# Optimization experiments

Measured on AMD Instinct MI355X. Metric: run time of the kernel, lower is better.

## Reference

```python
import jax, jax.numpy as jnp
import numpy as np

N = 8192      # nodes
E = 524288    # edges
F_IN = 256
H = 2         # heads
F_OUT = 128   # per-head out channels
LN_EPS = 1e-5
NEG_SLOPE = 0.2


def setup_inputs() -> dict:
    key = jax.random.key(0)
    ks = jax.random.split(key, 12)
    s = 0.05
    inp = {
        "x": jax.random.normal(ks[0], (N, F_IN), jnp.float32),
        "edge_index": jax.random.randint(ks[1], (2, E), 0, N, jnp.int32),
        "W_gat": jax.random.normal(ks[2], (F_IN, H * F_OUT), jnp.float32) * s,
        "att_src": jax.random.normal(ks[3], (H, F_OUT), jnp.float32) * s,
        "att_dst": jax.random.normal(ks[4], (H, F_OUT), jnp.float32) * s,
        "bias_gat": jnp.zeros((H * F_OUT,), jnp.float32),
        "w_a": jax.random.normal(ks[5], (256, 128), jnp.float32) * s,
        "b_a": jnp.zeros((128,), jnp.float32),
        "g_a": jnp.ones((128,), jnp.float32),
        "be_a": jnp.zeros((128,), jnp.float32),
        "w1": jax.random.normal(ks[6], (128, 64), jnp.float32) * s,
        "b1": jnp.zeros((64,), jnp.float32),
        "g1": jnp.ones((64,), jnp.float32),
        "be1": jnp.zeros((64,), jnp.float32),
        "w2": jax.random.normal(ks[7], (64, 32), jnp.float32) * s,
        "b2": jnp.zeros((32,), jnp.float32),
        "g2": jnp.ones((32,), jnp.float32),
        "be2": jnp.zeros((32,), jnp.float32),
        "w3": jax.random.normal(ks[8], (32, 3), jnp.float32) * s,
        "b3": jnp.zeros((3,), jnp.float32),
    }
    return inp


def _layernorm(x, g, b):
    mu = jnp.mean(x, axis=-1, keepdims=True)
    var = jnp.mean(jnp.square(x - mu), axis=-1, keepdims=True)
    return (x - mu) * jax.lax.rsqrt(var + LN_EPS) * g + b


def _gat_conv(x, edge_index, W, a_src, a_dst, bias):
    # PyG GATConv with add_self_loops=True, concat=True, dropout=0
    loop = jnp.arange(N, dtype=edge_index.dtype)
    src = jnp.concatenate([edge_index[0], loop])  # [E+N]
    dst = jnp.concatenate([edge_index[1], loop])
    h = (x @ W).reshape(N, H, F_OUT)              # per-node transform
    a_s = jnp.sum(h * a_src, axis=-1)             # [N,H]
    a_d = jnp.sum(h * a_dst, axis=-1)             # [N,H]
    e = jax.nn.leaky_relu(a_s[src] + a_d[dst], NEG_SLOPE)  # [E+N,H]
    # segment softmax over incoming edges of each dst node
    emax = jax.ops.segment_max(e, dst, num_segments=N)
    ex = jnp.exp(e - emax[dst])
    denom = jax.ops.segment_sum(ex, dst, num_segments=N)
    alpha = ex / (denom[dst] + 1e-16)             # [E+N,H]
    msg = h[src] * alpha[:, :, None]              # [E+N,H,F_OUT]
    out = jax.ops.segment_sum(msg, dst, num_segments=N)
    return out.reshape(N, H * F_OUT) + bias


def _safe_cdist(z):
    sq = jnp.sum(z * z, axis=-1)                  # [N]
    d2 = sq[:, None] + sq[None, :] - 2.0 * (z @ z.T)
    d2 = jnp.maximum(d2, 0.0)
    pos = d2 > 0
    return jnp.where(pos, jnp.sqrt(jnp.where(pos, d2, 1.0)), 0.0)


def reference(x, edge_index, W_gat, att_src, att_dst, bias_gat,
              w_a, b_a, g_a, be_a, w1, b1, g1, be1,
              w2, b2, g2, be2, w3, b3):
    h = _gat_conv(x, edge_index, W_gat, att_src, att_dst, bias_gat)
    h = jax.nn.relu(h)
    h = jax.nn.relu(_layernorm(h @ w_a + b_a, g_a, be_a))
    h = jax.nn.relu(_layernorm(h @ w1 + b1, g1, be1))
    h = jax.nn.relu(_layernorm(h @ w2 + b2, g2, be2))
    h = h @ w3 + b3                               # [N,3]
    return _safe_cdist(h)                         # [N,N]
```

## Files before the change

kernel.cpp:

```cpp
#include <hip/hip_runtime.h>
#include <hip/hip_bf16.h>

#define N_NODES 8192
#define E_EDGES 524288
#define F_IN    256
#define NH      2
#define F_OUT   128
#define C0      256

typedef float f32x4 __attribute__((ext_vector_type(4)));

__global__ __launch_bounds__(256) void gemm_xw_k(const float* __restrict__ A,
                                                 const float* __restrict__ B,
                                                 float* __restrict__ C) {
  const int K = 256, NC = 256;
  __shared__ float As[16][68];
  __shared__ float Bs[16][68];
  int bm = blockIdx.y * 64;
  int bn = blockIdx.x * 64;
  int tid = threadIdx.x;
  int tm = (tid >> 4) << 2;
  int tn = (tid & 15) << 2;
  float acc[4][4] = {};
  for (int k0 = 0; k0 < K; k0 += 16) {
#pragma unroll
    for (int i = 0; i < 4; i++) {
      int idx = tid + i * 256;
      int m = idx >> 4, k = idx & 15;
      As[k][m] = A[(bm + m) * K + k0 + k];
    }
#pragma unroll
    for (int i = 0; i < 4; i++) {
      int idx = tid + i * 256;
      int k = idx >> 6, n = idx & 63;
      Bs[k][n] = B[(k0 + k) * NC + bn + n];
    }
    __syncthreads();
#pragma unroll
    for (int k = 0; k < 16; k++) {
      float4 a = *(const float4*)&As[k][tm];
      float4 b = *(const float4*)&Bs[k][tn];
      acc[0][0] += a.x * b.x; acc[0][1] += a.x * b.y; acc[0][2] += a.x * b.z; acc[0][3] += a.x * b.w;
      acc[1][0] += a.y * b.x; acc[1][1] += a.y * b.y; acc[1][2] += a.y * b.z; acc[1][3] += a.y * b.w;
      acc[2][0] += a.z * b.x; acc[2][1] += a.z * b.y; acc[2][2] += a.z * b.z; acc[2][3] += a.z * b.w;
      acc[3][0] += a.w * b.x; acc[3][1] += a.w * b.y; acc[3][2] += a.w * b.z; acc[3][3] += a.w * b.w;
    }
    __syncthreads();
  }
#pragma unroll
  for (int i = 0; i < 4; i++) {
    float4 o = {acc[i][0], acc[i][1], acc[i][2], acc[i][3]};
    *(float4*)&C[(bm + tm + i) * NC + bn + tn] = o;
  }
}

__global__ __launch_bounds__(256) void att_scores_k(const float* __restrict__ h,
                                                    const float* __restrict__ att_src,
                                                    const float* __restrict__ att_dst,
                                                    float* __restrict__ a_s,
                                                    float* __restrict__ a_d) {
  int wave = threadIdx.x >> 6;
  int lane = threadIdx.x & 63;
  int node = blockIdx.x * 4 + wave;
  if (node >= N_NODES) return;
  const float4 hv = *(const float4*)(h + (size_t)node * C0 + lane * 4);
  const float4 vs = *(const float4*)(att_src + lane * 4);
  const float4 vd = *(const float4*)(att_dst + lane * 4);
  float s = hv.x * vs.x + hv.y * vs.y + hv.z * vs.z + hv.w * vs.w;
  float d = hv.x * vd.x + hv.y * vd.y + hv.z * vd.z + hv.w * vd.w;
#pragma unroll
  for (int off = 16; off; off >>= 1) {
    s += __shfl_xor(s, off);
    d += __shfl_xor(d, off);
  }
  if (lane == 0)  { a_s[node * 2] = s;     a_d[node * 2] = d; }
  if (lane == 32) { a_s[node * 2 + 1] = s; a_d[node * 2 + 1] = d; }
}

__global__ __launch_bounds__(256) void hist_k(const int* __restrict__ ei,
                                              int* __restrict__ deg) {
  int e = blockIdx.x * 256 + threadIdx.x;
  if (e < E_EDGES) atomicAdd(&deg[ei[E_EDGES + e]], 1);
}

__global__ __launch_bounds__(256) void scan_k(const int* __restrict__ deg,
                                              int* __restrict__ offs,
                                              int* __restrict__ cursor) {
  __shared__ int sums[256];
  int t = threadIdx.x;
  int local[32];
  int s = 0;
#pragma unroll
  for (int i = 0; i < 32; i++) { local[i] = s; s += deg[t * 32 + i]; }
  sums[t] = s;
  __syncthreads();
  for (int off = 1; off < 256; off <<= 1) {
    int u = (t >= off) ? sums[t - off] : 0;
    __syncthreads();
    if (t >= off) sums[t] += u;
    __syncthreads();
  }
  int base = sums[t] - s;
#pragma unroll
  for (int i = 0; i < 32; i++) {
    int o = base + local[i];
    offs[t * 32 + i] = o;
    cursor[t * 32 + i] = o;
  }
  if (t == 255) offs[N_NODES] = sums[255];
}

__global__ __launch_bounds__(256) void scatter_src_k(const int* __restrict__ ei,
                                                     int* __restrict__ cursor,
                                                     int* __restrict__ sorted_src) {
  int e = blockIdx.x * 256 + threadIdx.x;
  if (e < E_EDGES) {
    int d = ei[E_EDGES + e];
    int p = atomicAdd(&cursor[d], 1);
    sorted_src[p] = ei[e];
  }
}

__global__ __launch_bounds__(256) void gat_gather_k(const int* __restrict__ sorted_src,
                                                    const int* __restrict__ offs,
                                                    const float* __restrict__ h,
                                                    const float* __restrict__ a_s,
                                                    const float* __restrict__ a_d,
                                                    float* __restrict__ gat) {
  int wave = threadIdx.x >> 6;
  int lane = threadIdx.x & 63;
  int node = blockIdx.x * 4 + wave;
  if (node >= N_NODES) return;
  int start = offs[node], end = offs[node + 1];
  const float2 adv = *(const float2*)(a_d + node * 2);
  float ad0 = adv.x, ad1 = adv.y;
  int head = lane >> 5;
  float4 acc = {0, 0, 0, 0};
  float den0 = 0, den1 = 0;
  for (int base = start; base < end; base += 64) {
    int idx = base + lane;
    int s = -1;
    float e0 = 0, e1 = 0;
    if (idx < end) {
      s = sorted_src[idx];
      const float2 asv = *(const float2*)(a_s + s * 2);
      float v0 = asv.x + ad0; v0 = v0 > 0.0f ? v0 : 0.2f * v0;
      float v1 = asv.y + ad1; v1 = v1 > 0.0f ? v1 : 0.2f * v1;
      e0 = __expf(v0);
      e1 = __expf(v1);
      den0 += e0; den1 += e1;
    }
    int cnt = min(64, end - base);
    int j = 0;
    for (; j + 2 <= cnt; j += 2) {
      int sj0 = __shfl(s, j);
      int sj1 = __shfl(s, j + 1);
      float a00 = __shfl(e0, j),     a10 = __shfl(e1, j);
      float a01 = __shfl(e0, j + 1), a11 = __shfl(e1, j + 1);
      const float4 hv0 = *(const float4*)(h + (size_t)sj0 * C0 + lane * 4);
      const float4 hv1 = *(const float4*)(h + (size_t)sj1 * C0 + lane * 4);
      float w0 = head ? a10 : a00;
      float w1 = head ? a11 : a01;
      acc.x += hv0.x * w0; acc.y += hv0.y * w0; acc.z += hv0.z * w0; acc.w += hv0.w * w0;
      acc.x += hv1.x * w1; acc.y += hv1.y * w1; acc.z += hv1.z * w1; acc.w += hv1.w * w1;
    }
    if (j < cnt) {
      int sj = __shfl(s, j);
      float x0 = __shfl(e0, j);
      float x1 = __shfl(e1, j);
      float exh = head ? x1 : x0;
      const float4 hv = *(const float4*)(h + (size_t)sj * C0 + lane * 4);
      acc.x += hv.x * exh; acc.y += hv.y * exh;
      acc.z += hv.z * exh; acc.w += hv.w * exh;
    }
  }
  {
    const float2 asv = *(const float2*)(a_s + node * 2);
    float v0 = asv.x + ad0; v0 = v0 > 0.0f ? v0 : 0.2f * v0;
    float v1 = asv.y + ad1; v1 = v1 > 0.0f ? v1 : 0.2f * v1;
    float e0 = __expf(v0), e1 = __expf(v1);
    if (lane == 0) { den0 += e0; den1 += e1; }
    float exh = head ? e1 : e0;
    const float4 hv = *(const float4*)(h + (size_t)node * C0 + lane * 4);
    acc.x += hv.x * exh; acc.y += hv.y * exh;
    acc.z += hv.z * exh; acc.w += hv.w * exh;
  }
#pragma unroll
  for (int off = 32; off; off >>= 1) {
    den0 += __shfl_xor(den0, off);
    den1 += __shfl_xor(den1, off);
  }
  float denh = head ? den1 : den0;
  float inv = 1.0f / (denh + 1e-16f);
  float4 o = {acc.x * inv, acc.y * inv, acc.z * inv, acc.w * inv};
  *(float4*)(gat + (size_t)node * C0 + lane * 4) = o;
}

template <int KDIM, int ODIM, bool APPLY_IN>
__global__ __launch_bounds__(256) void fused_layer_k(const float* __restrict__ in,
                                                     const float* __restrict__ bias_in,
                                                     const float* __restrict__ W,
                                                     const float* __restrict__ b,
                                                     const float* __restrict__ g,
                                                     const float* __restrict__ be,
                                                     float* __restrict__ out) {
  const int TILE = 16;
  const int GROUPS = 256 / ODIM;
  const int NPT = TILE / GROUPS;
  __shared__ float in_t[TILE][KDIM + 4];
  __shared__ float out_t[TILE][ODIM + 1];
  int tid = threadIdx.x;
  int n0 = blockIdx.x * TILE;
  const int KD4 = KDIM / 4;
  for (int idx = tid; idx < TILE * KD4; idx += 256) {
    int n = idx / KD4, k4 = idx % KD4;
    float4 v = *(const float4*)&in[(size_t)(n0 + n) * KDIM + k4 * 4];
    if (APPLY_IN) {
      const float4 bb = *(const float4*)&bias_in[k4 * 4];
      v.x = fmaxf(v.x + bb.x, 0.0f);
      v.y = fmaxf(v.y + bb.y, 0.0f);
      v.z = fmaxf(v.z + bb.z, 0.0f);
      v.w = fmaxf(v.w + bb.w, 0.0f);
    }
    *(float4*)&in_t[n][k4 * 4] = v;
  }
  __syncthreads();
  int jj = tid % ODIM;
  int grp = tid / ODIM;
  float acc[NPT];
#pragma unroll
  for (int t = 0; t < NPT; t++) acc[t] = b[jj];
  for (int k = 0; k < KDIM; k += 4) {
    float w0 = W[(k + 0) * ODIM + jj];
    float w1 = W[(k + 1) * ODIM + jj];
    float w2 = W[(k + 2) * ODIM + jj];
    float w3 = W[(k + 3) * ODIM + jj];
#pragma unroll
    for (int t = 0; t < NPT; t++) {
      float4 v = *(const float4*)&in_t[grp + t * GROUPS][k];
      acc[t] = fmaf(v.w, w3, fmaf(v.z, w2, fmaf(v.y, w1, fmaf(v.x, w0, acc[t]))));
    }
  }
#pragma unroll
  for (int t = 0; t < NPT; t++) out_t[grp + t * GROUPS][jj] = acc[t];
  __syncthreads();
  const int TPN = 256 / TILE;
  const int JPT = ODIM / TPN;
  int node = tid / TPN;
  int ln = tid % TPN;
  float v[JPT];
  float s = 0;
#pragma unroll
  for (int q = 0; q < JPT; q++) { v[q] = out_t[node][ln + q * TPN]; s += v[q]; }
#pragma unroll
  for (int m = 1; m < TPN; m <<= 1) s += __shfl_xor(s, m);
  float mu = s / (float)ODIM;
  float vs = 0;
#pragma unroll
  for (int q = 0; q < JPT; q++) { float dd = v[q] - mu; vs += dd * dd; }
#pragma unroll
  for (int m = 1; m < TPN; m <<= 1) vs += __shfl_xor(vs, m);
  float inv = rsqrtf(vs / (float)ODIM + 1e-5f);
#pragma unroll
  for (int q = 0; q < JPT; q++) {
    int j = ln + q * TPN;
    float o = (v[q] - mu) * inv * g[j] + be[j];
    out[(size_t)(n0 + node) * ODIM + j] = fmaxf(o, 0.0f);
  }
}

__global__ __launch_bounds__(256) void final_z_k(const float* __restrict__ h2,
                                                 const float* __restrict__ w3,
                                                 const float* __restrict__ b3,
                                                 float* __restrict__ z) {
  int n = blockIdx.x * 256 + threadIdx.x;
  if (n >= N_NODES) return;
  float a0 = b3[0], a1 = b3[1], a2 = b3[2];
  const float4* row = (const float4*)(h2 + (size_t)n * 32);
#pragma unroll
  for (int q = 0; q < 8; q++) {
    float4 v = row[q];
    int k = q * 4;
    a0 += v.x * w3[(k + 0) * 3 + 0] + v.y * w3[(k + 1) * 3 + 0] + v.z * w3[(k + 2) * 3 + 0] + v.w * w3[(k + 3) * 3 + 0];
    a1 += v.x * w3[(k + 0) * 3 + 1] + v.y * w3[(k + 1) * 3 + 1] + v.z * w3[(k + 2) * 3 + 1] + v.w * w3[(k + 3) * 3 + 1];
    a2 += v.x * w3[(k + 0) * 3 + 2] + v.y * w3[(k + 1) * 3 + 2] + v.z * w3[(k + 2) * 3 + 2] + v.w * w3[(k + 3) * 3 + 2];
  }
  float4 zz = {a0, a1, a2, 0.0f};
  ((float4*)z)[n] = zz;
}

__global__ __launch_bounds__(256) void cdist_k(const float* __restrict__ z,
                                               float* __restrict__ out) {
  int i = blockIdx.x >> 3;
  int j0 = (((blockIdx.x & 7) << 8) + threadIdx.x) << 2;
  const float4 zi = ((const float4*)z)[i];
  f32x4 r;
  {
    float4 zj = ((const float4*)z)[j0 + 0];
    float dx = zi.x - zj.x, dy = zi.y - zj.y, dz = zi.z - zj.z;
    r.x = sqrtf(dx * dx + dy * dy + dz * dz);
  }
  {
    float4 zj = ((const float4*)z)[j0 + 1];
    float dx = zi.x - zj.x, dy = zi.y - zj.y, dz = zi.z - zj.z;
    r.y = sqrtf(dx * dx + dy * dy + dz * dz);
  }
  {
    float4 zj = ((const float4*)z)[j0 + 2];
    float dx = zi.x - zj.x, dy = zi.y - zj.y, dz = zi.z - zj.z;
    r.z = sqrtf(dx * dx + dy * dy + dz * dz);
  }
  {
    float4 zj = ((const float4*)z)[j0 + 3];
    float dx = zi.x - zj.x, dy = zi.y - zj.y, dz = zi.z - zj.z;
    r.w = sqrtf(dx * dx + dy * dy + dz * dz);
  }
  f32x4* dst = (f32x4*)out + (((size_t)i * N_NODES + j0) >> 2);
  __builtin_nontemporal_store(r, dst);
}

extern "C" void kernel_launch(void* const* d_in, const int* in_sizes, int n_in,
                              void* d_out, int out_size, void* d_ws, size_t ws_size,
                              hipStream_t stream) {
  const float* x        = (const float*)d_in[0];
  const int*   ei       = (const int*)d_in[1];
  const float* W_gat    = (const float*)d_in[2];
  const float* att_src  = (const float*)d_in[3];
  const float* att_dst  = (const float*)d_in[4];
  const float* bias_gat = (const float*)d_in[5];
  const float* w_a      = (const float*)d_in[6];
  const float* b_a      = (const float*)d_in[7];
  const float* g_a      = (const float*)d_in[8];
  const float* be_a     = (const float*)d_in[9];
  const float* w1       = (const float*)d_in[10];
  const float* b1       = (const float*)d_in[11];
  const float* g1       = (const float*)d_in[12];
  const float* be1      = (const float*)d_in[13];
  const float* w2       = (const float*)d_in[14];
  const float* b2       = (const float*)d_in[15];
  const float* g2       = (const float*)d_in[16];
  const float* be2      = (const float*)d_in[17];
  const float* w3       = (const float*)d_in[18];
  const float* b3       = (const float*)d_in[19];
  float* out = (float*)d_out;

  float* ws = (float*)d_ws;
  float* h     = ws;
  float* a_s   = h + 2097152;
  float* a_d   = a_s + 16384;
  float* gat   = a_d + 16384;
  float* hA    = gat + 2097152;
  float* h1    = hA + 1048576;
  float* h2    = h1 + 524288;
  float* z     = h2 + 262144;
  int*   deg    = (int*)(z + 32768);
  int*   offs   = deg + 8192;
  int*   cursor = offs + 8200;
  int*   sorted = cursor + 8192;

  hipMemsetAsync(deg, 0, N_NODES * sizeof(int), stream);

  gemm_xw_k<<<dim3(4, 128), 256, 0, stream>>>(x, W_gat, h);
  att_scores_k<<<2048, 256, 0, stream>>>(h, att_src, att_dst, a_s, a_d);
  hist_k<<<E_EDGES / 256, 256, 0, stream>>>(ei, deg);
  scan_k<<<1, 256, 0, stream>>>(deg, offs, cursor);
  scatter_src_k<<<E_EDGES / 256, 256, 0, stream>>>(ei, cursor, sorted);
  gat_gather_k<<<2048, 256, 0, stream>>>(sorted, offs, h, a_s, a_d, gat);
  fused_layer_k<256, 128, true><<<N_NODES / 16, 256, 0, stream>>>(gat, bias_gat, w_a, b_a, g_a, be_a, hA);
  fused_layer_k<128, 64, false><<<N_NODES / 16, 256, 0, stream>>>(hA, nullptr, w1, b1, g1, be1, h1);
  fused_layer_k<64, 32, false><<<N_NODES / 16, 256, 0, stream>>>(h1, nullptr, w2, b2, g2, be2, h2);
  final_z_k<<<N_NODES / 256, 256, 0, stream>>>(h2, w3, b3, z);
  cdist_k<<<N_NODES * 8, 256, 0, stream>>>(z, out);
}
```

Measured before the change: 484.8 us.

## Precompute edge attention exps in scatter and fuse final projection into last layer

The scatter kernel now handles self-loops as ordinary CSR entries, computes the leaky-relu exp weights per edge and stores them alongside the sorted source indices. The gather kernel then streams precomputed weights with wave-uniform loads instead of computing them per 64-edge chunk with shuffles, and it accumulates the denominator per lane without a reduction. Separately, the final 32-to-3 projection is fused into the last fused_layer kernel, which removes the h2 buffer and one launch. This costs an extra per-edge float2 write and read, and the gather loop now issues scalar-indexed loads serially.

```diff
diff --git a/kernel.cpp b/kernel.cpp
--- a/kernel.cpp
+++ b/kernel.cpp
@@ -7,6 +7,7 @@
 #define NH      2
 #define F_OUT   128
 #define C0      256
+#define E_TOT   (E_EDGES + N_NODES)
 
 typedef float f32x4 __attribute__((ext_vector_type(4)));
 
@@ -91,7 +92,7 @@
   int local[32];
   int s = 0;
 #pragma unroll
-  for (int i = 0; i < 32; i++) { local[i] = s; s += deg[t * 32 + i]; }
+  for (int i = 0; i < 32; i++) { local[i] = s; s += deg[t * 32 + i] + 1; }
   sums[t] = s;
   __syncthreads();
   for (int off = 1; off < 256; off <<= 1) {
@@ -110,100 +111,81 @@
   if (t == 255) offs[N_NODES] = sums[255];
 }
 
-__global__ __launch_bounds__(256) void scatter_src_k(const int* __restrict__ ei,
-                                                     int* __restrict__ cursor,
-                                                     int* __restrict__ sorted_src) {
+__global__ __launch_bounds__(256) void scatter_k(const int* __restrict__ ei,
+                                                 const float* __restrict__ a_s,
+                                                 const float* __restrict__ a_d,
+                                                 int* __restrict__ cursor,
+                                                 int* __restrict__ sorted_src,
+                                                 float2* __restrict__ exv) {
   int e = blockIdx.x * 256 + threadIdx.x;
-  if (e < E_EDGES) {
-    int d = ei[E_EDGES + e];
-    int p = atomicAdd(&cursor[d], 1);
-    sorted_src[p] = ei[e];
-  }
+  if (e >= E_TOT) return;
+  int s, d;
+  if (e < E_EDGES) { s = ei[e]; d = ei[E_EDGES + e]; }
+  else             { s = d = e - E_EDGES; }
+  const float2 as = ((const float2*)a_s)[s];
+  const float2 ad = ((const float2*)a_d)[d];
+  float v0 = as.x + ad.x; v0 = v0 > 0.0f ? v0 : 0.2f * v0;
+  float v1 = as.y + ad.y; v1 = v1 > 0.0f ? v1 : 0.2f * v1;
+  int p = atomicAdd(&cursor[d], 1);
+  sorted_src[p] = s;
+  exv[p] = make_float2(__expf(v0), __expf(v1));
 }
 
 __global__ __launch_bounds__(256) void gat_gather_k(const int* __restrict__ sorted_src,
+                                                    const float2* __restrict__ exv,
                                                     const int* __restrict__ offs,
                                                     const float* __restrict__ h,
-                                                    const float* __restrict__ a_s,
-                                                    const float* __restrict__ a_d,
                                                     float* __restrict__ gat) {
   int wave = threadIdx.x >> 6;
   int lane = threadIdx.x & 63;
   int node = blockIdx.x * 4 + wave;
   if (node >= N_NODES) return;
-  int start = offs[node], end = offs[node + 1];
-  const float2 adv = *(const float2*)(a_d + node * 2);
-  float ad0 = adv.x, ad1 = adv.y;
+  int start = __builtin_amdgcn_readfirstlane(offs[node]);
+  int end   = __builtin_amdgcn_readfirstlane(offs[node + 1]);
   int head = lane >> 5;
   float4 acc = {0, 0, 0, 0};
-  float den0 = 0, den1 = 0;
-  for (int base = start; base < end; base += 64) {
-    int idx = base + lane;
-    int s = -1;
-    float e0 = 0, e1 = 0;
-    if (idx < end) {
-      s = sorted_src[idx];
-      const float2 asv = *(const float2*)(a_s + s * 2);
-      float v0 = asv.x + ad0; v0 = v0 > 0.0f ? v0 : 0.2f * v0;
-      float v1 = asv.y + ad1; v1 = v1 > 0.0f ? v1 : 0.2f * v1;
-      e0 = __expf(v0);
-      e1 = __expf(v1);
-      den0 += e0; den1 += e1;
-    }
-    int cnt = min(64, end - base);
-    int j = 0;
-    for (; j + 2 <= cnt; j += 2) {
-      int sj0 = __shfl(s, j);
-      int sj1 = __shfl(s, j + 1);
-      float a00 = __shfl(e0, j),     a10 = __shfl(e1, j);
-      float a01 = __shfl(e0, j + 1), a11 = __shfl(e1, j + 1);
-      const float4 hv0 = *(const float4*)(h + (size_t)sj0 * C0 + lane * 4);
-      const float4 hv1 = *(const float4*)(h + (size_t)sj1 * C0 + lane * 4);
-      float w0 = head ? a10 : a00;
-      float w1 = head ? a11 : a01;
-      acc.x += hv0.x * w0; acc.y += hv0.y * w0; acc.z += hv0.z * w0; acc.w += hv0.w * w0;
-      acc.x += hv1.x * w1; acc.y += hv1.y * w1; acc.z += hv1.z * w1; acc.w += hv1.w * w1;
-    }
-    if (j < cnt) {
-      int sj = __shfl(s, j);
-      float x0 = __shfl(e0, j);
-      float x1 = __shfl(e1, j);
-      float exh = head ? x1 : x0;
-      const float4 hv = *(const float4*)(h + (size_t)sj * C0 + lane * 4);
-      acc.x += hv.x * exh; acc.y += hv.y * exh;
-      acc.z += hv.z * exh; acc.w += hv.w * exh;
-    }
-  }
-  {
-    const float2 asv = *(const float2*)(a_s + node * 2);
-    float v0 = asv.x + ad0; v0 = v0 > 0.0f ? v0 : 0.2f * v0;
-    float v1 = asv.y + ad1; v1 = v1 > 0.0f ? v1 : 0.2f * v1;
-    float e0 = __expf(v0), e1 = __expf(v1);
-    if (lane == 0) { den0 += e0; den1 += e1; }
-    float exh = head ? e1 : e0;
-    const float4 hv = *(const float4*)(h + (size_t)node * C0 + lane * 4);
-    acc.x += hv.x * exh; acc.y += hv.y * exh;
-    acc.z += hv.z * exh; acc.w += hv.w * exh;
-  }
-#pragma unroll
-  for (int off = 32; off; off >>= 1) {
-    den0 += __shfl_xor(den0, off);
-    den1 += __shfl_xor(den1, off);
-  }
-  float denh = head ? den1 : den0;
-  float inv = 1.0f / (denh + 1e-16f);
+  float den = 0.0f;
+  int e = start;
+  for (; e + 2 <= end; e += 2) {
+    int s0 = sorted_src[e];
+    int s1 = sorted_src[e + 1];
+    float2 x0 = exv[e];
+    float2 x1 = exv[e + 1];
+    const float4 hv0 = *(const float4*)(h + (size_t)s0 * C0 + lane * 4);
+    const float4 hv1 = *(const float4*)(h + (size_t)s1 * C0 + lane * 4);
+    float w0 = head ? x0.y : x0.x;
+    float w1 = head ? x1.y : x1.x;
+    den += w0; den += w1;
+    acc.x = fmaf(hv0.x, w0, acc.x); acc.y = fmaf(hv0.y, w0, acc.y);
+    acc.z = fmaf(hv0.z, w0, acc.z); acc.w = fmaf(hv0.w, w0, acc.w);
+    acc.x = fmaf(hv1.x, w1, acc.x); acc.y = fmaf(hv1.y, w1, acc.y);
+    acc.z = fmaf(hv1.z, w1, acc.z); acc.w = fmaf(hv1.w, w1, acc.w);
+  }
+  if (e < end) {
+    int s0 = sorted_src[e];
+    float2 x0 = exv[e];
+    const float4 hv0 = *(const float4*)(h + (size_t)s0 * C0 + lane * 4);
+    float w0 = head ? x0.y : x0.x;
+    den += w0;
+    acc.x = fmaf(hv0.x, w0, acc.x); acc.y = fmaf(hv0.y, w0, acc.y);
+    acc.z = fmaf(hv0.z, w0, acc.z); acc.w = fmaf(hv0.w, w0, acc.w);
+  }
+  float inv = 1.0f / (den + 1e-16f);
   float4 o = {acc.x * inv, acc.y * inv, acc.z * inv, acc.w * inv};
   *(float4*)(gat + (size_t)node * C0 + lane * 4) = o;
 }
 
-template <int KDIM, int ODIM, bool APPLY_IN>
+template <int KDIM, int ODIM, bool APPLY_IN, bool FUSE_Z>
 __global__ __launch_bounds__(256) void fused_layer_k(const float* __restrict__ in,
                                                      const float* __restrict__ bias_in,
                                                      const float* __restrict__ W,
                                                      const float* __restrict__ b,
                                                      const float* __restrict__ g,
                                                      const float* __restrict__ be,
-                                                     float* __restrict__ out) {
+                                                     float* __restrict__ out,
+                                                     const float* __restrict__ w3,
+                                                     const float* __restrict__ b3,
+                                                     float* __restrict__ zout) {
   const int TILE = 16;
   const int GROUPS = 256 / ODIM;
   const int NPT = TILE / GROUPS;
@@ -234,11 +216,11 @@
     float w0 = W[(k + 0) * ODIM + jj];
     float w1 = W[(k + 1) * ODIM + jj];
     float w2 = W[(k + 2) * ODIM + jj];
-    float w3 = W[(k + 3) * ODIM + jj];
+    float w3v = W[(k + 3) * ODIM + jj];
 #pragma unroll
     for (int t = 0; t < NPT; t++) {
       float4 v = *(const float4*)&in_t[grp + t * GROUPS][k];
-      acc[t] = fmaf(v.w, w3, fmaf(v.z, w2, fmaf(v.y, w1, fmaf(v.x, w0, acc[t]))));
+      acc[t] = fmaf(v.w, w3v, fmaf(v.z, w2, fmaf(v.y, w1, fmaf(v.x, w0, acc[t]))));
     }
   }
 #pragma unroll
@@ -261,32 +243,34 @@
 #pragma unroll
   for (int m = 1; m < TPN; m <<= 1) vs += __shfl_xor(vs, m);
   float inv = rsqrtf(vs / (float)ODIM + 1e-5f);
-#pragma unroll
-  for (int q = 0; q < JPT; q++) {
-    int j = ln + q * TPN;
-    float o = (v[q] - mu) * inv * g[j] + be[j];
-    out[(size_t)(n0 + node) * ODIM + j] = fmaxf(o, 0.0f);
-  }
-}
-
-__global__ __launch_bounds__(256) void final_z_k(const float* __restrict__ h2,
-                                                 const float* __restrict__ w3,
-                                                 const float* __restrict__ b3,
-                                                 float* __restrict__ z) {
-  int n = blockIdx.x * 256 + threadIdx.x;
-  if (n >= N_NODES) return;
-  float a0 = b3[0], a1 = b3[1], a2 = b3[2];
-  const float4* row = (const float4*)(h2 + (size_t)n * 32);
-#pragma unroll
-  for (int q = 0; q < 8; q++) {
-    float4 v = row[q];
-    int k = q * 4;
-    a0 += v.x * w3[(k + 0) * 3 + 0] + v.y * w3[(k + 1) * 3 + 0] + v.z * w3[(k + 2) * 3 + 0] + v.w * w3[(k + 3) * 3 + 0];
-    a1 += v.x * w3[(k + 0) * 3 + 1] + v.y * w3[(k + 1) * 3 + 1] + v.z * w3[(k + 2) * 3 + 1] + v.w * w3[(k + 3) * 3 + 1];
-    a2 += v.x * w3[(k + 0) * 3 + 2] + v.y * w3[(k + 1) * 3 + 2] + v.z * w3[(k + 2) * 3 + 2] + v.w * w3[(k + 3) * 3 + 2];
-  }
-  float4 zz = {a0, a1, a2, 0.0f};
-  ((float4*)z)[n] = zz;
+  if (FUSE_Z) {
+    float p0 = 0, p1 = 0, p2 = 0;
+#pragma unroll
+    for (int q = 0; q < JPT; q++) {
+      int j = ln + q * TPN;
+      float val = fmaxf((v[q] - mu) * inv * g[j] + be[j], 0.0f);
+      p0 = fmaf(val, w3[j * 3 + 0], p0);
+      p1 = fmaf(val, w3[j * 3 + 1], p1);
+      p2 = fmaf(val, w3[j * 3 + 2], p2);
+    }
+#pragma unroll
+    for (int m = 1; m < TPN; m <<= 1) {
+      p0 += __shfl_xor(p0, m);
+      p1 += __shfl_xor(p1, m);
+      p2 += __shfl_xor(p2, m);
+    }
+    if (ln == 0) {
+      float4 zz = {p0 + b3[0], p1 + b3[1], p2 + b3[2], 0.0f};
+      ((float4*)zout)[n0 + node] = zz;
+    }
+  } else {
+#pragma unroll
+    for (int q = 0; q < JPT; q++) {
+      int j = ln + q * TPN;
+      float o = (v[q] - mu) * inv * g[j] + be[j];
+      out[(size_t)(n0 + node) * ODIM + j] = fmaxf(o, 0.0f);
+    }
+  }
 }
 
 __global__ __launch_bounds__(256) void cdist_k(const float* __restrict__ z,
@@ -345,18 +329,18 @@
   float* out = (float*)d_out;
 
   float* ws = (float*)d_ws;
-  float* h     = ws;
-  float* a_s   = h + 2097152;
-  float* a_d   = a_s + 16384;
-  float* gat   = a_d + 16384;
-  float* hA    = gat + 2097152;
-  float* h1    = hA + 1048576;
-  float* h2    = h1 + 524288;
-  float* z     = h2 + 262144;
-  int*   deg    = (int*)(z + 32768);
-  int*   offs   = deg + 8192;
-  int*   cursor = offs + 8200;
-  int*   sorted = cursor + 8192;
+  float*  h      = ws;
+  float*  a_s    = h + 2097152;
+  float*  a_d    = a_s + 16384;
+  float*  gat    = a_d + 16384;
+  float*  hA     = gat + 2097152;
+  float*  h1     = hA + 1048576;
+  float*  z      = h1 + 524288;
+  float2* exv    = (float2*)(z + 32768);
+  int*    deg    = (int*)(exv + E_TOT);
+  int*    offs   = deg + 8192;
+  int*    cursor = offs + 8200;
+  int*    sorted = cursor + 8192;
 
   hipMemsetAsync(deg, 0, N_NODES * sizeof(int), stream);
 
@@ -364,11 +348,10 @@
   att_scores_k<<<2048, 256, 0, stream>>>(h, att_src, att_dst, a_s, a_d);
   hist_k<<<E_EDGES / 256, 256, 0, stream>>>(ei, deg);
   scan_k<<<1, 256, 0, stream>>>(deg, offs, cursor);
-  scatter_src_k<<<E_EDGES / 256, 256, 0, stream>>>(ei, cursor, sorted);
-  gat_gather_k<<<2048, 256, 0, stream>>>(sorted, offs, h, a_s, a_d, gat);
-  fused_layer_k<256, 128, true><<<N_NODES / 16, 256, 0, stream>>>(gat, bias_gat, w_a, b_a, g_a, be_a, hA);
-  fused_layer_k<128, 64, false><<<N_NODES / 16, 256, 0, stream>>>(hA, nullptr, w1, b1, g1, be1, h1);
-  fused_layer_k<64, 32, false><<<N_NODES / 16, 256, 0, stream>>>(h1, nullptr, w2, b2, g2, be2, h2);
-  final_z_k<<<N_NODES / 256, 256, 0, stream>>>(h2, w3, b3, z);
+  scatter_k<<<E_TOT / 256, 256, 0, stream>>>(ei, a_s, a_d, cursor, sorted, exv);
+  gat_gather_k<<<2048, 256, 0, stream>>>(sorted, exv, offs, h, gat);
+  fused_layer_k<256, 128, true,  false><<<N_NODES / 16, 256, 0, stream>>>(gat, bias_gat, w_a, b_a, g_a, be_a, hA, nullptr, nullptr, nullptr);
+  fused_layer_k<128, 64,  false, false><<<N_NODES / 16, 256, 0, stream>>>(hA, nullptr, w1, b1, g1, be1, h1, nullptr, nullptr, nullptr);
+  fused_layer_k<64,  32,  false, true ><<<N_NODES / 16, 256, 0, stream>>>(h1, nullptr, w2, b2, g2, be2, nullptr, w3, b3, z);
   cdist_k<<<N_NODES * 8, 256, 0, stream>>>(z, out);
 }
```

New measurement: 481.9 us. About the same (-0.6%).
